# Performance work log

Hardware: AMD Instinct MI355X
Metric: run time of the kernel (lower is better)

Reference implementation:

```python
import jax, jax.numpy as jnp
import numpy as np

PATCH = (160, 160, 160)  # patch_size from init_kwargs


def _zero_centered_mesh(patch):
    # create_zero_centered_coordinate_mesh: meshgrid(range(p), indexing='ij') - (p-1)/2
    axes = [jnp.arange(p, dtype=jnp.float32) - (p - 1) / 2.0 for p in patch]
    return jnp.stack(jnp.meshgrid(*axes, indexing='ij'), axis=0)  # [3, *patch]


def setup_inputs() -> dict:
    key = jax.random.key(0)
    k1, k2 = jax.random.split(key)
    data = jax.random.normal(k1, (4, 2, 192, 192, 192), dtype=jnp.float32)
    seg = jax.random.randint(k2, (4, 2, 192, 192, 192), 0, 4).astype(jnp.float32)
    return {"data": data, "seg": seg}


def reference(data, seg):
    B, C, D, H, W = data.shape
    patch = PATCH
    # zero-centered coordinate mesh, shifted to the center of the input volume
    coords = _zero_centered_mesh(patch)  # [3, pD, pH, pW]
    ctr = jnp.array([(D - 1) / 2.0, (H - 1) / 2.0, (W - 1) / 2.0], dtype=jnp.float32)
    coords = coords + ctr[:, None, None, None]
    coord_list = [coords[0], coords[1], coords[2]]

    # map_coordinates-style resampling of every (b, c) volume at the mesh points
    vols = data.reshape(B * C, D, H, W)
    interp = jax.vmap(
        lambda v: jax.scipy.ndimage.map_coordinates(
            v, coord_list, order=1, mode="constant", cval=0.0
        )
    )
    data_out = interp(vols).reshape(B, C, *patch)

    # center crop of seg (crop_type='center'): lbs = (shape - crop_size) // 2
    lbs = [(s - p) // 2 for s, p in zip((D, H, W), patch)]
    seg_out = seg[
        :,
        :,
        lbs[0] : lbs[0] + patch[0],
        lbs[1] : lbs[1] + patch[1],
        lbs[2] : lbs[2] + patch[2],
    ]
    return data_out, seg_out
```

## Files before the change

kernel.cpp:

```cpp
#include <hip/hip_runtime.h>


constexpr unsigned P   = 160;
constexpr unsigned S   = 192;
constexpr unsigned OFF = 16;
constexpr unsigned BC  = 8;
constexpr unsigned ROW4 = P / 4;
constexpr unsigned OUT4 = BC * P * P * ROW4;

using f4 = __attribute__((ext_vector_type(4))) float;

__global__ __launch_bounds__(256) void crop_copy_kernel(
    const f4* __restrict__ data,
    const f4* __restrict__ seg,
    f4* __restrict__ out)
{
    unsigned o = blockIdx.x * 256u + threadIdx.x;

    unsigned w4  = o % ROW4;
    unsigned row = o / ROW4;
    unsigned h   = row % P;
    unsigned t   = row / P;
    unsigned d   = t % P;
    unsigned bc  = t / P;

    unsigned src = (bc * (S * S * S) + (d + OFF) * (S * S) + (h + OFF) * S + OFF) / 4u + w4;

    f4 a = __builtin_nontemporal_load(&data[src]);
    f4 b = __builtin_nontemporal_load(&seg[src]);
    __builtin_nontemporal_store(a, &out[o]);
    __builtin_nontemporal_store(b, &out[o + OUT4]);
}

extern "C" void kernel_launch(void* const* d_in, const int* in_sizes, int n_in,
                              void* d_out, int out_size, void* d_ws, size_t ws_size,
                              hipStream_t stream)
{
    const f4* data = (const f4*)d_in[0];
    const f4* seg  = (const f4*)d_in[1];
    f4* out = (f4*)d_out;

    constexpr unsigned block = 256;
    constexpr unsigned grid  = OUT4 / block;
    crop_copy_kernel<<<grid, block, 0, stream>>>(data, seg, out);
}
```

Measured before the change: 485.0 us.

## Map one block per output plane and batch eight row loads per thread

The crop copy now launches one 320-thread block per (batch-channel, depth) plane. Each thread walks 40 rows in five iterations and issues eight independent 16-byte loads, four from data and four from seg, before writing them out. This removes the per-element div/mod index math and raises the number of memory requests in flight per thread to better hide latency. Loads switch from nontemporal to ordinary cached loads while stores stay nontemporal. The larger per-thread register footprint and fewer resident waves are the trade-off.

```diff
diff --git a/kernel.cpp b/kernel.cpp
--- a/kernel.cpp
+++ b/kernel.cpp
@@ -1,35 +1,55 @@
 #include <hip/hip_runtime.h>
 
 
-constexpr unsigned P   = 160;
-constexpr unsigned S   = 192;
-constexpr unsigned OFF = 16;
-constexpr unsigned BC  = 8;
-constexpr unsigned ROW4 = P / 4;
-constexpr unsigned OUT4 = BC * P * P * ROW4;
+constexpr unsigned P      = 160;
+constexpr unsigned S      = 192;
+constexpr unsigned OFF    = 16;
+constexpr unsigned BC     = 8;
+constexpr unsigned ROW4   = P / 4;
+constexpr unsigned SROW4  = S / 4;
+constexpr unsigned SPLANE4= S * S / 4;
+constexpr unsigned SVOL4  = S * S * S / 4;
+constexpr unsigned OUT4   = BC * P * P * ROW4;
 
 using f4 = __attribute__((ext_vector_type(4))) float;
 
-__global__ __launch_bounds__(256) void crop_copy_kernel(
+__global__ __launch_bounds__(320) void crop_copy_kernel(
     const f4* __restrict__ data,
     const f4* __restrict__ seg,
     f4* __restrict__ out)
 {
-    unsigned o = blockIdx.x * 256u + threadIdx.x;
+    const unsigned t  = threadIdx.x;
+    const unsigned h0 = t / ROW4;
+    const unsigned w4 = t - h0 * ROW4;
+    const unsigned bc = blockIdx.x / P;
+    const unsigned d  = blockIdx.x - bc * P;
 
-    unsigned w4  = o % ROW4;
-    unsigned row = o / ROW4;
-    unsigned h   = row % P;
-    unsigned t   = row / P;
-    unsigned d   = t % P;
-    unsigned bc  = t / P;
+    unsigned src = bc * SVOL4 + (d + OFF) * SPLANE4 + (h0 + OFF) * SROW4
+                 + (OFF / 4) + w4;
+    unsigned o   = blockIdx.x * (P * ROW4) + h0 * ROW4 + w4;
 
-    unsigned src = (bc * (S * S * S) + (d + OFF) * (S * S) + (h + OFF) * S + OFF) / 4u + w4;
+    for (unsigned g = 0; g < 5; ++g) {
+        f4 a0 = data[src];
+        f4 a1 = data[src +  8 * SROW4];
+        f4 a2 = data[src + 16 * SROW4];
+        f4 a3 = data[src + 24 * SROW4];
+        f4 b0 = seg[src];
+        f4 b1 = seg[src +  8 * SROW4];
+        f4 b2 = seg[src + 16 * SROW4];
+        f4 b3 = seg[src + 24 * SROW4];
 
-    f4 a = __builtin_nontemporal_load(&data[src]);
-    f4 b = __builtin_nontemporal_load(&seg[src]);
-    __builtin_nontemporal_store(a, &out[o]);
-    __builtin_nontemporal_store(b, &out[o + OUT4]);
+        __builtin_nontemporal_store(a0, &out[o]);
+        __builtin_nontemporal_store(a1, &out[o +  8 * ROW4]);
+        __builtin_nontemporal_store(a2, &out[o + 16 * ROW4]);
+        __builtin_nontemporal_store(a3, &out[o + 24 * ROW4]);
+        __builtin_nontemporal_store(b0, &out[o + OUT4]);
+        __builtin_nontemporal_store(b1, &out[o + OUT4 +  8 * ROW4]);
+        __builtin_nontemporal_store(b2, &out[o + OUT4 + 16 * ROW4]);
+        __builtin_nontemporal_store(b3, &out[o + OUT4 + 24 * ROW4]);
+
+        src += 32 * SROW4;
+        o   += 32 * ROW4;
+    }
 }
 
 extern "C" void kernel_launch(void* const* d_in, const int* in_sizes, int n_in,
@@ -40,7 +60,7 @@
     const f4* seg  = (const f4*)d_in[1];
     f4* out = (f4*)d_out;
 
-    constexpr unsigned block = 256;
-    constexpr unsigned grid  = OUT4 / block;
+    constexpr unsigned block = 320;
+    constexpr unsigned grid  = BC * P;
     crop_copy_kernel<<<grid, block, 0, stream>>>(data, seg, out);
 }
```

Result: slower. 524.7 us (+8.2%).
